# Optimization experiments

Measured on AMD Instinct MI355X. Metric: run time of the kernel, lower is better.

Reference implementation:

```python
import jax, jax.numpy as jnp
import numpy as np

B, D, O, E = 8192, 1024, 1024, 8

def setup_inputs() -> dict:
    key = jax.random.key(0)
    ks = jax.random.split(key, 5)
    s = 1.0 / np.sqrt(D)
    return {
        "x": jax.random.normal(ks[0], (B, D), dtype=jnp.float32),
        "Wg": jax.random.uniform(ks[1], (D, E), jnp.float32, -s, s),
        "bg": jax.random.uniform(ks[2], (E,), jnp.float32, -s, s),
        "We": jax.random.uniform(ks[3], (E, D, O), jnp.float32, -s, s),
        "be": jax.random.uniform(ks[4], (E, O), jnp.float32, -s, s),
    }

def reference(x, Wg, bg, We, be):
    # gating: [B, E], softmax over experts (dim=1)
    gates = jax.nn.softmax(x @ Wg + bg, axis=1)
    # dense expert outputs: [B, E, O] (single batched GEMM over all experts)
    expert_out = jnp.einsum('bd,edo->beo', x, We) + be[None, :, :]
    # softmax-weighted combine (bmm of [B,1,E] @ [B,E,O] -> [B,O])
    return jnp.einsum('be,beo->bo', gates, expert_out)
```

## Files before the change

### kernel.cpp

```cpp
#include <hip/hip_runtime.h>
#include <hip/hip_bf16.h>
#include <stdint.h>

#define B_SZ 8192
#define D_SZ 1024
#define O_SZ 1024
#define E_SZ 8

typedef __bf16 bf16_t;
typedef __bf16 bf16x8 __attribute__((ext_vector_type(8)));
typedef __bf16 bf16x4 __attribute__((ext_vector_type(4)));
typedef float  f32x4  __attribute__((ext_vector_type(4)));

__global__ __launch_bounds__(256) void prep_kernel(
    const float* __restrict__ x, const float* __restrict__ Wg,
    const float* __restrict__ bg, const float* __restrict__ We,
    float* __restrict__ gates, bf16_t* __restrict__ xb,
    bf16_t* __restrict__ WeT) {
  __shared__ float tile[64][65];
  const int tid = threadIdx.x;
  if (blockIdx.x < 2048) {
    const int w = tid >> 6, lane = tid & 63;
    const int b = blockIdx.x * 4 + w;
    const float* xr = x + (size_t)b * D_SZ;
    float acc[8];
#pragma unroll
    for (int e = 0; e < 8; ++e) acc[e] = 0.f;
    float xs[16];
#pragma unroll
    for (int it = 0; it < 4; ++it) {
      const int d = it * 256 + lane * 4;
      float4 xv = *(const float4*)(xr + d);
      xs[it * 4 + 0] = xv.x; xs[it * 4 + 1] = xv.y;
      xs[it * 4 + 2] = xv.z; xs[it * 4 + 3] = xv.w;
#pragma unroll
      for (int j = 0; j < 4; ++j) {
        const float4* wr = (const float4*)(Wg + (size_t)(d + j) * 8);
        float4 w0 = wr[0], w1 = wr[1];
        float xj = xs[it * 4 + j];
        acc[0] += xj * w0.x; acc[1] += xj * w0.y;
        acc[2] += xj * w0.z; acc[3] += xj * w0.w;
        acc[4] += xj * w1.x; acc[5] += xj * w1.y;
        acc[6] += xj * w1.z; acc[7] += xj * w1.w;
      }
    }
#pragma unroll
    for (int off = 32; off >= 1; off >>= 1) {
#pragma unroll
      for (int e = 0; e < 8; ++e) acc[e] += __shfl_xor(acc[e], off, 64);
    }
    float g[8];
#pragma unroll
    for (int e = 0; e < 8; ++e) g[e] = acc[e] + bg[e];
    float m = g[0];
#pragma unroll
    for (int e = 1; e < 8; ++e) m = fmaxf(m, g[e]);
    float s = 0.f;
#pragma unroll
    for (int e = 0; e < 8; ++e) { g[e] = __expf(g[e] - m); s += g[e]; }
    float inv = 1.0f / s;
    if (lane == 0) {
      float* gr = gates + (size_t)b * 8;
#pragma unroll
      for (int e = 0; e < 8; ++e) gr[e] = g[e] * inv;
    }
    bf16_t* ar = xb + (size_t)b * D_SZ;
#pragma unroll
    for (int it = 0; it < 4; ++it) {
      const int d = it * 256 + lane * 4;
      bf16x4 ov;
      ov[0] = (bf16_t)xs[it * 4 + 0]; ov[1] = (bf16_t)xs[it * 4 + 1];
      ov[2] = (bf16_t)xs[it * 4 + 2]; ov[3] = (bf16_t)xs[it * 4 + 3];
      *(bf16x4*)(ar + d) = ov;
    }
  } else {
    const int tb = blockIdx.x - 2048;
    const int e = tb >> 8, rem = tb & 255;
    const int d0 = (rem >> 4) << 6, o0 = (rem & 15) << 6;
    const float* src = We + (size_t)e * D_SZ * O_SZ + (size_t)d0 * O_SZ + o0;
#pragma unroll
    for (int p = 0; p < 4; ++p) {
      const int d = p * 16 + (tid >> 4);
      const int o = (tid & 15) * 4;
      float4 v = *(const float4*)(src + (size_t)d * O_SZ + o);
      tile[d][o] = v.x; tile[d][o + 1] = v.y;
      tile[d][o + 2] = v.z; tile[d][o + 3] = v.w;
    }
    __syncthreads();
    bf16_t* dstp = WeT + (size_t)e * O_SZ * D_SZ + (size_t)o0 * D_SZ + d0;
#pragma unroll
    for (int p = 0; p < 2; ++p) {
      const int o = p * 32 + (tid >> 3);
      const int d8 = (tid & 7) * 8;
      bf16x8 ov;
#pragma unroll
      for (int k = 0; k < 8; ++k) ov[k] = (bf16_t)tile[d8 + k][o];
      *(bf16x8*)(dstp + (size_t)o * D_SZ + d8) = ov;
    }
  }
}

__device__ __forceinline__ void gload_lds16(const bf16_t* g, char* l) {
  __builtin_amdgcn_global_load_lds(
      (const __attribute__((address_space(1))) void*)g,
      (__attribute__((address_space(3))) void*)l, 16, 0, 0);
}

__global__ __launch_bounds__(256, 2) void moe_gemm(
    const bf16_t* __restrict__ xb,
    const bf16_t* __restrict__ wet,
    const float* __restrict__ gates,
    const float* __restrict__ be,
    float* __restrict__ out)
{
  __shared__ bf16_t lA[128 * 32];
  __shared__ bf16_t lB[128 * 32];
  __shared__ float  lG[128 * 8];

  const int tid = threadIdx.x;
  const int b0 = blockIdx.y * 128;
  const int o0 = blockIdx.x * 128;

  {
    const float* gsrc = gates + (size_t)b0 * 8;
#pragma unroll
    for (int i = 0; i < 4; ++i) lG[tid + 256 * i] = gsrc[tid + 256 * i];
  }

  const int w = tid >> 6;
  const int lane = tid & 63;
  const int wm = (w >> 1) * 64;
  const int wn = (w & 1) * 64;
  const int m16 = lane & 15;
  const int q = lane >> 4;

  const int gi0 = tid, gi1 = tid + 256;
  const int ar0 = gi0 >> 2, ac0 = (((gi0 & 3) ^ ((gi0 >> 3) & 3)) * 8);
  const int ar1 = gi1 >> 2, ac1 = (((gi1 & 3) ^ ((gi1 >> 3) & 3)) * 8);
  char* lA0 = (char*)lA + w * 64 * 16;
  char* lA1 = (char*)lA + (256 + w * 64) * 16;
  char* lB0 = (char*)lB + w * 64 * 16;
  char* lB1 = (char*)lB + (256 + w * 64) * 16;

  const bf16_t* Abase = xb + (size_t)b0 * D_SZ;

  f32x4 outAcc[4][4];
#pragma unroll
  for (int i = 0; i < 4; ++i)
#pragma unroll
    for (int j = 0; j < 4; ++j) outAcc[i][j] = f32x4{0.f, 0.f, 0.f, 0.f};

  for (int e = 0; e < E_SZ; ++e) {
    const bf16_t* Bbase = wet + ((size_t)e * O_SZ + o0) * D_SZ;
    f32x4 acc[4][4];
#pragma unroll
    for (int i = 0; i < 4; ++i)
#pragma unroll
      for (int j = 0; j < 4; ++j) acc[i][j] = f32x4{0.f, 0.f, 0.f, 0.f};

    for (int kt = 0; kt < D_SZ / 32; ++kt) {
      const int kc = kt * 32;
      __syncthreads();
      gload_lds16(Abase + (size_t)ar0 * D_SZ + kc + ac0, lA0);
      gload_lds16(Abase + (size_t)ar1 * D_SZ + kc + ac1, lA1);
      gload_lds16(Bbase + (size_t)ar0 * D_SZ + kc + ac0, lB0);
      gload_lds16(Bbase + (size_t)ar1 * D_SZ + kc + ac1, lB1);
      __syncthreads();

      bf16x8 af[4], bfr[4];
#pragma unroll
      for (int i = 0; i < 4; ++i) {
        int r = wm + i * 16 + m16;
        int pg = (q ^ ((r >> 1) & 3)) * 8;
        af[i] = *(const bf16x8*)&lA[r * 32 + pg];
      }
#pragma unroll
      for (int j = 0; j < 4; ++j) {
        int r = wn + j * 16 + m16;
        int pg = (q ^ ((r >> 1) & 3)) * 8;
        bfr[j] = *(const bf16x8*)&lB[r * 32 + pg];
      }
#pragma unroll
      for (int i = 0; i < 4; ++i)
#pragma unroll
        for (int j = 0; j < 4; ++j)
          acc[i][j] = __builtin_amdgcn_mfma_f32_16x16x32_bf16(
              af[i], bfr[j], acc[i][j], 0, 0, 0);
    }

#pragma unroll
    for (int j = 0; j < 4; ++j) {
      float bec = be[e * O_SZ + o0 + wn + j * 16 + m16];
#pragma unroll
      for (int i = 0; i < 4; ++i) {
#pragma unroll
        for (int rg = 0; rg < 4; ++rg) {
          float gv = lG[(wm + i * 16 + q * 4 + rg) * 8 + e];
          outAcc[i][j][rg] += gv * (acc[i][j][rg] + bec);
        }
      }
    }
  }

#pragma unroll
  for (int i = 0; i < 4; ++i)
#pragma unroll
    for (int rg = 0; rg < 4; ++rg) {
      float* orow = out + (size_t)(b0 + wm + i * 16 + q * 4 + rg) * O_SZ
                    + o0 + wn + m16;
#pragma unroll
      for (int j = 0; j < 4; ++j) orow[j * 16] = outAcc[i][j][rg];
    }
}

extern "C" void kernel_launch(void* const* d_in, const int* in_sizes, int n_in,
                              void* d_out, int out_size, void* d_ws, size_t ws_size,
                              hipStream_t stream) {
  const float* x  = (const float*)d_in[0];
  const float* Wg = (const float*)d_in[1];
  const float* bg = (const float*)d_in[2];
  const float* We = (const float*)d_in[3];
  const float* be = (const float*)d_in[4];
  float* out = (float*)d_out;

  char* ws = (char*)d_ws;
  float*  gates = (float*)ws;
  bf16_t* xb    = (bf16_t*)(ws + (1 << 18));
  bf16_t* wet   = (bf16_t*)(ws + (1 << 18) + (1 << 24));

  prep_kernel<<<4096, 256, 0, stream>>>(x, Wg, bg, We, gates, xb, wet);
  moe_gemm<<<dim3(O_SZ / 128, B_SZ / 128), 256, 0, stream>>>(
      xb, wet, gates, be, out);
}
```

Baseline: 308.5 us.

## Double-buffer LDS tiles and prefetch the next K-stage across experts

The expert and K loops are flattened into one 256-stage loop. Each stage issues the async global-to-LDS loads for the next stage into the other half of a double-buffered LDS tile, then waits only on the older loads with raw s_barrier and vmcnt. This lets memory transfers overlap MFMA work instead of fully serialising load and compute behind two __syncthreads per step. The cost is doubled LDS for A/B tiles and reliance on hand-written waitcnt and barrier ordering. The last stage redundantly reloads into the buffer being read, which is benign only because the data is identical.

Result: slower. 319.3 us (+3.5%).

```diff
diff --git a/kernel.cpp b/kernel.cpp
--- a/kernel.cpp
+++ b/kernel.cpp
@@ -106,6 +106,10 @@
       (__attribute__((address_space(3))) void*)l, 16, 0, 0);
 }
 
+#define RAW_BARRIER() asm volatile("s_barrier" ::: "memory")
+#define WAIT_VM4()    asm volatile("s_waitcnt vmcnt(4)" ::: "memory")
+#define WAIT_LGKM0()  asm volatile("s_waitcnt lgkmcnt(0)" ::: "memory")
+
 __global__ __launch_bounds__(256, 2) void moe_gemm(
     const bf16_t* __restrict__ xb,
     const bf16_t* __restrict__ wet,
@@ -113,8 +117,8 @@
     const float* __restrict__ be,
     float* __restrict__ out)
 {
-  __shared__ bf16_t lA[128 * 32];
-  __shared__ bf16_t lB[128 * 32];
+  __shared__ bf16_t lA[2][128 * 32];
+  __shared__ bf16_t lB[2][128 * 32];
   __shared__ float  lG[128 * 8];
 
   const int tid = threadIdx.x;
@@ -137,12 +141,11 @@
   const int gi0 = tid, gi1 = tid + 256;
   const int ar0 = gi0 >> 2, ac0 = (((gi0 & 3) ^ ((gi0 >> 3) & 3)) * 8);
   const int ar1 = gi1 >> 2, ac1 = (((gi1 & 3) ^ ((gi1 >> 3) & 3)) * 8);
-  char* lA0 = (char*)lA + w * 64 * 16;
-  char* lA1 = (char*)lA + (256 + w * 64) * 16;
-  char* lB0 = (char*)lB + w * 64 * 16;
-  char* lB1 = (char*)lB + (256 + w * 64) * 16;
+  const int la0off = (w * 64) * 16;
+  const int la1off = (256 + w * 64) * 16;
 
   const bf16_t* Abase = xb + (size_t)b0 * D_SZ;
+  const bf16_t* Wbase = wet + (size_t)o0 * D_SZ;
 
   f32x4 outAcc[4][4];
 #pragma unroll
@@ -150,53 +153,74 @@
 #pragma unroll
     for (int j = 0; j < 4; ++j) outAcc[i][j] = f32x4{0.f, 0.f, 0.f, 0.f};
 
-  for (int e = 0; e < E_SZ; ++e) {
-    const bf16_t* Bbase = wet + ((size_t)e * O_SZ + o0) * D_SZ;
-    f32x4 acc[4][4];
+  WAIT_LGKM0();
+  RAW_BARRIER();
+
+  {
+    const bf16_t* Bb = Wbase;
+    gload_lds16(Abase + (size_t)ar0 * D_SZ + ac0, (char*)lA[0] + la0off);
+    gload_lds16(Abase + (size_t)ar1 * D_SZ + ac1, (char*)lA[0] + la1off);
+    gload_lds16(Bb + (size_t)ar0 * D_SZ + ac0, (char*)lB[0] + la0off);
+    gload_lds16(Bb + (size_t)ar1 * D_SZ + ac1, (char*)lB[0] + la1off);
+  }
+
+  f32x4 acc[4][4];
+#pragma unroll
+  for (int i = 0; i < 4; ++i)
+#pragma unroll
+    for (int j = 0; j < 4; ++j) acc[i][j] = f32x4{0.f, 0.f, 0.f, 0.f};
+
+  for (int s = 0; s < E_SZ * (D_SZ / 32); ++s) {
+    const int e = s >> 5;
+    const int par = s & 1;
+
+    RAW_BARRIER();
+    {
+      const int sn = (s < 255) ? s + 1 : 255;
+      const int en = sn >> 5, kn = (sn & 31) * 32;
+      const int pn = sn & 1;
+      const bf16_t* An = Abase + kn;
+      const bf16_t* Bn = Wbase + (size_t)en * (O_SZ * D_SZ) + kn;
+      gload_lds16(An + (size_t)ar0 * D_SZ + ac0, (char*)lA[pn] + la0off);
+      gload_lds16(An + (size_t)ar1 * D_SZ + ac1, (char*)lA[pn] + la1off);
+      gload_lds16(Bn + (size_t)ar0 * D_SZ + ac0, (char*)lB[pn] + la0off);
+      gload_lds16(Bn + (size_t)ar1 * D_SZ + ac1, (char*)lB[pn] + la1off);
+    }
+    WAIT_VM4();
+    RAW_BARRIER();
+
+    bf16x8 af[4], bfr[4];
+#pragma unroll
+    for (int i = 0; i < 4; ++i) {
+      int r = wm + i * 16 + m16;
+      int pg = (q ^ ((r >> 1) & 3)) * 8;
+      af[i] = *(const bf16x8*)&lA[par][r * 32 + pg];
+    }
+#pragma unroll
+    for (int j = 0; j < 4; ++j) {
+      int r = wn + j * 16 + m16;
+      int pg = (q ^ ((r >> 1) & 3)) * 8;
+      bfr[j] = *(const bf16x8*)&lB[par][r * 32 + pg];
+    }
 #pragma unroll
     for (int i = 0; i < 4; ++i)
 #pragma unroll
-      for (int j = 0; j < 4; ++j) acc[i][j] = f32x4{0.f, 0.f, 0.f, 0.f};
-
-    for (int kt = 0; kt < D_SZ / 32; ++kt) {
-      const int kc = kt * 32;
-      __syncthreads();
-      gload_lds16(Abase + (size_t)ar0 * D_SZ + kc + ac0, lA0);
-      gload_lds16(Abase + (size_t)ar1 * D_SZ + kc + ac1, lA1);
-      gload_lds16(Bbase + (size_t)ar0 * D_SZ + kc + ac0, lB0);
-      gload_lds16(Bbase + (size_t)ar1 * D_SZ + kc + ac1, lB1);
-      __syncthreads();
-
-      bf16x8 af[4], bfr[4];
-#pragma unroll
-      for (int i = 0; i < 4; ++i) {
-        int r = wm + i * 16 + m16;
-        int pg = (q ^ ((r >> 1) & 3)) * 8;
-        af[i] = *(const bf16x8*)&lA[r * 32 + pg];
-      }
+      for (int j = 0; j < 4; ++j)
+        acc[i][j] = __builtin_amdgcn_mfma_f32_16x16x32_bf16(
+            af[i], bfr[j], acc[i][j], 0, 0, 0);
+
+    if ((s & 31) == 31) {
 #pragma unroll
       for (int j = 0; j < 4; ++j) {
-        int r = wn + j * 16 + m16;
-        int pg = (q ^ ((r >> 1) & 3)) * 8;
-        bfr[j] = *(const bf16x8*)&lB[r * 32 + pg];
-      }
-#pragma unroll
-      for (int i = 0; i < 4; ++i)
-#pragma unroll
-        for (int j = 0; j < 4; ++j)
-          acc[i][j] = __builtin_amdgcn_mfma_f32_16x16x32_bf16(
-              af[i], bfr[j], acc[i][j], 0, 0, 0);
-    }
-
-#pragma unroll
-    for (int j = 0; j < 4; ++j) {
-      float bec = be[e * O_SZ + o0 + wn + j * 16 + m16];
-#pragma unroll
-      for (int i = 0; i < 4; ++i) {
-#pragma unroll
-        for (int rg = 0; rg < 4; ++rg) {
-          float gv = lG[(wm + i * 16 + q * 4 + rg) * 8 + e];
-          outAcc[i][j][rg] += gv * (acc[i][j][rg] + bec);
+        float bec = be[e * O_SZ + o0 + wn + j * 16 + m16];
+#pragma unroll
+        for (int i = 0; i < 4; ++i) {
+#pragma unroll
+          for (int rg = 0; rg < 4; ++rg) {
+            float gv = lG[(wm + i * 16 + q * 4 + rg) * 8 + e];
+            outAcc[i][j][rg] += gv * (acc[i][j][rg] + bec);
+            acc[i][j][rg] = 0.f;
+          }
         }
       }
     }
```
